# Kernel optimization log

Measured on AMD Instinct MI355X. Metric: run time of the kernel, lower is better.

## Reference

```python
import jax, jax.numpy as jnp
import numpy as np

OFF_THRESH = 0.5  # stand-in for specials.OFF_THRESH


def _smap3x3(x_value, y_value, z_value, r_mask, key_query):
    B, C = x_value.shape[0], x_value.shape[1]
    H, W = x_value.shape[-2], x_value.shape[-1]
    dt = x_value.dtype

    z_values = z_value.reshape(B, C, 1, H, W)
    r_m = r_mask.reshape(B, C, 1, H, W)
    x_z = jnp.concatenate([x_value, y_value, z_value], axis=2)  # [B,C,3,H,W]

    # argmin over the 3x3 window dim -> one-hot selection mask [B,C,9,H,W]
    ind = jnp.argmin(key_query, axis=2)                      # [B,C,H,W]
    w = jnp.moveaxis(jax.nn.one_hot(ind, 9, dtype=dt), -1, 2)  # [B,C,9,H,W]

    valid = (r_m > OFF_THRESH) & (z_values > 0.0)            # [B,C,1,H,W]
    w = jnp.where(valid, w, jnp.zeros((), dt))

    center = jnp.zeros((9,), dt).at[4].set(1.0).reshape(1, 1, 9, 1, 1)
    bad = (r_m > OFF_THRESH) & ~(z_values > 0.0)
    # torch.where(1 - bad > 0.5, w, temp) == where(bad, center, w)
    w = jnp.where(bad, center, w)

    wd = jax.lax.stop_gradient(w).reshape(B, C, 3, 3, H, W)
    # outer product over window (s,t) and xyz (z) dims -> [B,C,3,3,3,H,W]
    new_xz = jnp.einsum('bcsthw,bczhw->bcstzhw', wd, x_z)

    w2 = jnp.where(valid, w, center)
    new_r = (jax.lax.stop_gradient(w2) * r_m).reshape(B, C, 3, 3, 1, H, W)

    return jnp.concatenate([new_xz, new_r], axis=4)  # [B,C,3,3,4,H,W]


def setup_inputs() -> dict:
    key = jax.random.key(0)
    k1, k2, k3, k4, k5 = jax.random.split(key, 5)
    B, C, H, W = 4, 1, 480, 640
    return {
        "x_value": jax.random.normal(k1, (B, C, 1, H, W), dtype=jnp.float32),
        "y_value": jax.random.normal(k2, (B, C, 1, H, W), dtype=jnp.float32),
        "z_value": jax.random.normal(k3, (B, C, 1, H, W), dtype=jnp.float32),
        "r_mask": jax.random.uniform(k4, (B, C, 1, H, W), dtype=jnp.float32),
        "key_query": jax.random.normal(k5, (B, C, 9, H, W), dtype=jnp.float32),
    }


def reference(x_value, y_value, z_value, r_mask, key_query):
    return _smap3x3(x_value, y_value, z_value, r_mask, key_query)
```

## Files before the change

### kernel.cpp

```cpp
#include <hip/hip_runtime.h>


constexpr int H = 480;
constexpr int W = 640;
constexpr int HW = H * W;
constexpr int HW4 = HW / 4;
constexpr int BLK = 256;
constexpr int GRIDX = HW4 / BLK;

typedef __attribute__((ext_vector_type(4))) float fvec4;

__device__ __forceinline__ fvec4 nt_load4(const fvec4* p) {
    return __builtin_nontemporal_load(p);
}

__global__ __launch_bounds__(256) void smap3x3_kernel(
    const fvec4* __restrict__ x,
    const fvec4* __restrict__ y,
    const fvec4* __restrict__ z,
    const fvec4* __restrict__ r,
    const fvec4* __restrict__ kq,
    fvec4* __restrict__ out)
{
    const int hw4 = blockIdx.x * BLK + threadIdx.x;
    const int b   = blockIdx.y;
    const size_t pix = (size_t)b * HW4 + hw4;

    const fvec4* kqb = kq + (size_t)b * 9 * HW4 + hw4;
    fvec4 best = nt_load4(kqb);
    int i0 = 0, i1 = 0, i2 = 0, i3 = 0;
#pragma unroll
    for (int k = 1; k < 9; ++k) {
        const fvec4 kk = nt_load4(kqb + (size_t)k * HW4);
        if (kk.x < best.x) { best.x = kk.x; i0 = k; }
        if (kk.y < best.y) { best.y = kk.y; i1 = k; }
        if (kk.z < best.z) { best.z = kk.z; i2 = k; }
        if (kk.w < best.w) { best.w = kk.w; i3 = k; }
    }

    const fvec4 xv = nt_load4(x + pix);
    const fvec4 yv = nt_load4(y + pix);
    const fvec4 zv = nt_load4(z + pix);
    const fvec4 rv = nt_load4(r + pix);

    int sw0, sw1, sw2, sw3;
    int s20, s21, s22, s23;
    { const bool ron = rv.x > 0.5f, zon = zv.x > 0.0f;
      sw0 = ron ? (zon ? i0 : 4) : -1;  s20 = (ron && zon) ? i0 : 4; }
    { const bool ron = rv.y > 0.5f, zon = zv.y > 0.0f;
      sw1 = ron ? (zon ? i1 : 4) : -1;  s21 = (ron && zon) ? i1 : 4; }
    { const bool ron = rv.z > 0.5f, zon = zv.z > 0.0f;
      sw2 = ron ? (zon ? i2 : 4) : -1;  s22 = (ron && zon) ? i2 : 4; }
    { const bool ron = rv.w > 0.5f, zon = zv.w > 0.0f;
      sw3 = ron ? (zon ? i3 : 4) : -1;  s23 = (ron && zon) ? i3 : 4; }

    fvec4* outb = out + (size_t)b * 36 * HW4 + hw4;
#pragma unroll
    for (int k = 0; k < 9; ++k) {
        fvec4 ox, oy, oz, orr;
        const bool m0 = (k == sw0), m1 = (k == sw1), m2 = (k == sw2), m3 = (k == sw3);
        ox.x = m0 ? xv.x : 0.0f;  ox.y = m1 ? xv.y : 0.0f;
        ox.z = m2 ? xv.z : 0.0f;  ox.w = m3 ? xv.w : 0.0f;
        oy.x = m0 ? yv.x : 0.0f;  oy.y = m1 ? yv.y : 0.0f;
        oy.z = m2 ? yv.z : 0.0f;  oy.w = m3 ? yv.w : 0.0f;
        oz.x = m0 ? zv.x : 0.0f;  oz.y = m1 ? zv.y : 0.0f;
        oz.z = m2 ? zv.z : 0.0f;  oz.w = m3 ? zv.w : 0.0f;
        orr.x = (k == s20) ? rv.x : 0.0f;  orr.y = (k == s21) ? rv.y : 0.0f;
        orr.z = (k == s22) ? rv.z : 0.0f;  orr.w = (k == s23) ? rv.w : 0.0f;

        outb[(size_t)(4 * k + 0) * HW4] = ox;
        outb[(size_t)(4 * k + 1) * HW4] = oy;
        outb[(size_t)(4 * k + 2) * HW4] = oz;
        outb[(size_t)(4 * k + 3) * HW4] = orr;
    }
}

extern "C" void kernel_launch(void* const* d_in, const int* in_sizes, int n_in,
                              void* d_out, int out_size, void* d_ws, size_t ws_size,
                              hipStream_t stream) {
    const fvec4* x  = (const fvec4*)d_in[0];
    const fvec4* y  = (const fvec4*)d_in[1];
    const fvec4* z  = (const fvec4*)d_in[2];
    const fvec4* r  = (const fvec4*)d_in[3];
    const fvec4* kq = (const fvec4*)d_in[4];
    fvec4* out = (fvec4*)d_out;

    dim3 grid(GRIDX, 4);
    smap3x3_kernel<<<grid, dim3(BLK), 0, stream>>>(x, y, z, r, kq, out);
}
```

Measured before the change: 228.8 us.

## Split into selection kernel and per-plane scatter kernel with packed byte selectors

Splits the work into two kernels. The first computes the argmin and validity logic once and stores a packed byte selector per pixel in the workspace. The second writes each of the 36 output planes as a contiguous chunked stream with nontemporal stores, so the scattered writes across 36 planes per thread become sequential per-block writes. In exchange it adds a second launch, a workspace round trip, and a reread of the inputs up to nine times per plane. The fused kernel is kept as a fallback when no workspace is available.

```diff
diff --git a/kernel.cpp b/kernel.cpp
--- a/kernel.cpp
+++ b/kernel.cpp
@@ -5,16 +5,100 @@
 constexpr int W = 640;
 constexpr int HW = H * W;
 constexpr int HW4 = HW / 4;
+constexpr int NB = 4;
 constexpr int BLK = 256;
 constexpr int GRIDX = HW4 / BLK;
+
+constexpr int CHUNKS = 10;
+constexpr int CHUNK_F4 = HW4 / CHUNKS;
+constexpr int ITERS = CHUNK_F4 / BLK;
 
 typedef __attribute__((ext_vector_type(4))) float fvec4;
 
 __device__ __forceinline__ fvec4 nt_load4(const fvec4* p) {
     return __builtin_nontemporal_load(p);
 }
+__device__ __forceinline__ void nt_store4(fvec4* p, fvec4 v) {
+    __builtin_nontemporal_store(v, p);
+}
 
-__global__ __launch_bounds__(256) void smap3x3_kernel(
+__device__ __forceinline__ unsigned char pack_sel(float rr, float zz, int i) {
+    const bool ron = rr > 0.5f, zon = zz > 0.0f;
+    const int sw = ron ? (zon ? i : 4) : 15;
+    const int s2 = (ron && zon) ? i : 4;
+    return (unsigned char)(sw | (s2 << 4));
+}
+
+__global__ __launch_bounds__(256) void smap_sel_kernel(
+    const fvec4* __restrict__ z,
+    const fvec4* __restrict__ r,
+    const fvec4* __restrict__ kq,
+    uchar4* __restrict__ sel)
+{
+    const int hw4 = blockIdx.x * BLK + threadIdx.x;
+    const int b   = blockIdx.y;
+    const size_t pix = (size_t)b * HW4 + hw4;
+
+    const fvec4* kqb = kq + (size_t)b * 9 * HW4 + hw4;
+    fvec4 best = nt_load4(kqb);
+    int i0 = 0, i1 = 0, i2 = 0, i3 = 0;
+#pragma unroll
+    for (int k = 1; k < 9; ++k) {
+        const fvec4 kk = nt_load4(kqb + (size_t)k * HW4);
+        if (kk.x < best.x) { best.x = kk.x; i0 = k; }
+        if (kk.y < best.y) { best.y = kk.y; i1 = k; }
+        if (kk.z < best.z) { best.z = kk.z; i2 = k; }
+        if (kk.w < best.w) { best.w = kk.w; i3 = k; }
+    }
+
+    const fvec4 zv = z[pix];
+    const fvec4 rv = r[pix];
+
+    uchar4 s;
+    s.x = pack_sel(rv.x, zv.x, i0);
+    s.y = pack_sel(rv.y, zv.y, i1);
+    s.z = pack_sel(rv.z, zv.z, i2);
+    s.w = pack_sel(rv.w, zv.w, i3);
+    sel[pix] = s;
+}
+
+__global__ __launch_bounds__(256) void smap_scatter_kernel(
+    const fvec4* __restrict__ x,
+    const fvec4* __restrict__ y,
+    const fvec4* __restrict__ z,
+    const fvec4* __restrict__ r,
+    const uchar4* __restrict__ sel,
+    fvec4* __restrict__ out)
+{
+    const int p     = blockIdx.x;
+    const int chunk = blockIdx.y;
+    const int b     = blockIdx.z;
+    const int k = p >> 2;
+    const int c = p & 3;
+
+    const fvec4* val = (c == 0) ? x : (c == 1) ? y : (c == 2) ? z : r;
+    const int shift = (c < 3) ? 0 : 4;
+
+    const size_t base = (size_t)b * HW4 + (size_t)chunk * CHUNK_F4;
+    const uchar4* sb = sel + base;
+    const fvec4*  vb = val + base;
+    fvec4* ob = out + ((size_t)b * 36 + p) * HW4 + (size_t)chunk * CHUNK_F4;
+
+#pragma unroll 6
+    for (int it = 0; it < ITERS; ++it) {
+        const int idx = it * BLK + threadIdx.x;
+        const uchar4 s = sb[idx];
+        const fvec4  v = vb[idx];
+        fvec4 o;
+        o.x = (((s.x >> shift) & 15) == k) ? v.x : 0.0f;
+        o.y = (((s.y >> shift) & 15) == k) ? v.y : 0.0f;
+        o.z = (((s.z >> shift) & 15) == k) ? v.z : 0.0f;
+        o.w = (((s.w >> shift) & 15) == k) ? v.w : 0.0f;
+        nt_store4(ob + idx, o);
+    }
+}
+
+__global__ __launch_bounds__(256) void smap3x3_fused_kernel(
     const fvec4* __restrict__ x,
     const fvec4* __restrict__ y,
     const fvec4* __restrict__ z,
@@ -43,8 +127,7 @@
     const fvec4 zv = nt_load4(z + pix);
     const fvec4 rv = nt_load4(r + pix);
 
-    int sw0, sw1, sw2, sw3;
-    int s20, s21, s22, s23;
+    int sw0, sw1, sw2, sw3, s20, s21, s22, s23;
     { const bool ron = rv.x > 0.5f, zon = zv.x > 0.0f;
       sw0 = ron ? (zon ? i0 : 4) : -1;  s20 = (ron && zon) ? i0 : 4; }
     { const bool ron = rv.y > 0.5f, zon = zv.y > 0.0f;
@@ -85,6 +168,15 @@
     const fvec4* kq = (const fvec4*)d_in[4];
     fvec4* out = (fvec4*)d_out;
 
-    dim3 grid(GRIDX, 4);
-    smap3x3_kernel<<<grid, dim3(BLK), 0, stream>>>(x, y, z, r, kq, out);
+    const size_t sel_bytes = (size_t)NB * HW;
+
+    if (d_ws != nullptr && ws_size >= sel_bytes) {
+        uchar4* sel = (uchar4*)d_ws;
+        smap_sel_kernel<<<dim3(GRIDX, NB), dim3(BLK), 0, stream>>>(z, r, kq, sel);
+        smap_scatter_kernel<<<dim3(36, CHUNKS, NB), dim3(BLK), 0, stream>>>(
+            x, y, z, r, sel, out);
+    } else {
+        smap3x3_fused_kernel<<<dim3(GRIDX, NB), dim3(BLK), 0, stream>>>(
+            x, y, z, r, kq, out);
+    }
 }
```

Measured after the change: 254.2 us. 11.1% more time.
